# Optimization experiments

Measured on AMD Instinct MI355X. Metric: run time of the kernel, lower is better.

The kernel has to match this reference:

```python
import jax, jax.numpy as jnp
import numpy as np

R, S, D, V, K, B, L, U, I = 20000, 64, 128, 50000, 32, 2048, 20480, 100000, 100000


def setup_inputs() -> dict:
    key = jax.random.key(0)
    ks = jax.random.split(key, 16)
    # segment ids: equal-sized history per batch element (guaranteed non-empty)
    seg = (jnp.arange(L, dtype=jnp.int32) // (L // B)).astype(jnp.int32)
    return {
        "user": jax.random.randint(ks[0], (B,), 0, U, dtype=jnp.int32),
        "item": jax.random.randint(ks[1], (B,), 0, I, dtype=jnp.int32),
        "historical_review": jax.random.randint(ks[2], (R, S), 0, V, dtype=jnp.int32),
        "historical_review_positive": jax.random.normal(ks[3], (R, D), jnp.float32),
        "user_hist_idx": jax.random.randint(ks[4], (L,), 0, R, dtype=jnp.int32),
        "user_hist_seg": seg,
        "item_hist_idx": jax.random.randint(ks[5], (L,), 0, R, dtype=jnp.int32),
        "item_hist_seg": seg,
        "word_emb": jax.random.normal(ks[6], (V, D), jnp.float32) * 0.02,
        "M_w": jax.random.normal(ks[7], (D, D), jnp.float32) * (1.0 / np.sqrt(D)),
        "M_b": jnp.zeros((D,), jnp.float32),
        "W_w": jax.random.normal(ks[8], (D, K), jnp.float32) * (1.0 / np.sqrt(D)),
        "W_b": jnp.zeros((K,), jnp.float32),
        "T_w": jax.random.normal(ks[9], (K, D), jnp.float32) * (1.0 / np.sqrt(K)),
        "T_b": jnp.zeros((D,), jnp.float32),
        "user_emb": jax.random.normal(ks[10], (U, D), jnp.float32) * 0.02,
        "item_emb": jax.random.normal(ks[11], (I, D), jnp.float32) * 0.02,
        "avg_rating": jnp.full((1,), 3.5, jnp.float32),
    }


def _segment_mean(x, seg, num_segments):
    s = jax.ops.segment_sum(x, seg, num_segments=num_segments)
    c = jax.ops.segment_sum(jnp.ones(seg.shape, x.dtype), seg, num_segments=num_segments)
    return s / jnp.maximum(c, 1.0)[:, None]


def reference(user, item, historical_review, historical_review_positive,
              user_hist_idx, user_hist_seg, item_hist_idx, item_hist_seg,
              word_emb, M_w, M_b, W_w, W_b, T_w, T_b,
              user_emb, item_emb, avg_rating):
    # --- aspect extraction (ABAE-style) over R historical reviews ---
    e_w = word_emb[historical_review]                      # [R, S, D] gather
    y_s = historical_review_positive                       # [R, D] sentence embedding
    # dx = transform_M(e_w) @ y_s  -> attention logits over words
    dx = jnp.einsum('rsd,de,re->rs', e_w, M_w, y_s) + jnp.einsum('d,rd->r', M_b, y_s)[:, None]
    ax = jax.nn.softmax(dx, axis=1)                        # [R, S]
    z_s = jnp.einsum('rsd,rs->rd', e_w, ax)                # [R, D]
    p_t = jax.nn.softmax(z_s @ W_w + W_b, axis=1)          # [R, K] aspect probs
    r_s = p_t @ T_w + T_b                                  # [R, D] aspect-based review embedding
    # --- ragged gather + mean-pool over user/item histories ---
    ua = _segment_mean(r_s[user_hist_idx], user_hist_seg, B)  # [B, D]
    ia = _segment_mean(r_s[item_hist_idx], item_hist_seg, B)  # [B, D]
    uf = user_emb[user]                                    # [B, D]
    itf = item_emb[item]                                   # [B, D]
    prediction = jnp.sum(ua * ia, axis=-1) + jnp.sum(uf * itf, axis=-1) + avg_rating[0]
    return prediction  # [B]
```

## Files before the change

### kernel.cpp

```cpp
#include <hip/hip_runtime.h>


typedef __attribute__((ext_vector_type(8))) short bf16x8;
typedef __attribute__((ext_vector_type(4))) float f32x4;
typedef __attribute__((ext_vector_type(2))) float vf2;

__device__ __forceinline__ unsigned int f2bf_rne(float x) {
  unsigned int u = __float_as_uint(x);
  return (u + 0x7fffu + ((u >> 16) & 1u)) >> 16;
}

__global__ __launch_bounds__(256) void kA_mfma(
    const float* __restrict__ We, const float* __restrict__ Mw,
    const float* __restrict__ Ww, unsigned char* __restrict__ Z,
    int V, int ntiles) {
  __shared__ uint4 Bs[2560];
  int t = threadIdx.x;
  int L = t & 63, wid = t >> 6;

#pragma unroll
  for (int q = 0; q < 10; ++q) {
    int c = t + q * 256;
    int cl = c & 63, g = c >> 6;
    int jt = g >> 2, ks = g & 3;
    int n = jt * 16 + (cl & 15);
    int k0 = ks * 32 + (cl >> 4) * 8;
    float v[8];
#pragma unroll
    for (int j = 0; j < 8; ++j) {
      int e = k0 + j;
      v[j] = (n < 128) ? Mw[(size_t)e * 128 + n] : Ww[(size_t)e * 32 + (n - 128)];
    }
    uint4 pk;
    pk.x = f2bf_rne(v[0]) | (f2bf_rne(v[1]) << 16);
    pk.y = f2bf_rne(v[2]) | (f2bf_rne(v[3]) << 16);
    pk.z = f2bf_rne(v[4]) | (f2bf_rne(v[5]) << 16);
    pk.w = f2bf_rne(v[6]) | (f2bf_rne(v[7]) << 16);
    Bs[c] = pk;
  }
  __syncthreads();

  for (int tile = blockIdx.x; tile < ntiles; tile += gridDim.x) {
    int r0 = tile * 64;
    if (r0 > V - 64) r0 = V - 64;
    int rowA = r0 + wid * 16 + (L & 15);
    const float4* Arow = (const float4*)(We + (size_t)rowA * 128);

    f32x4 acc[10];
#pragma unroll
    for (int jt = 0; jt < 10; ++jt) acc[jt] = (f32x4){0.f, 0.f, 0.f, 0.f};

#pragma unroll
    for (int ks = 0; ks < 4; ++ks) {
      int koff4 = ks * 8 + (L >> 4) * 2;
      float4 a0 = Arow[koff4];
      float4 a1 = Arow[koff4 + 1];
      union { uint4 u; bf16x8 v; } A;
      A.u.x = f2bf_rne(a0.x) | (f2bf_rne(a0.y) << 16);
      A.u.y = f2bf_rne(a0.z) | (f2bf_rne(a0.w) << 16);
      A.u.z = f2bf_rne(a1.x) | (f2bf_rne(a1.y) << 16);
      A.u.w = f2bf_rne(a1.z) | (f2bf_rne(a1.w) << 16);
#pragma unroll
      for (int jt = 0; jt < 10; ++jt) {
        union { uint4 u; bf16x8 v; } Bf;
        Bf.u = Bs[(jt * 4 + ks) * 64 + L];
        acc[jt] = __builtin_amdgcn_mfma_f32_16x16x32_bf16(A.v, Bf.v, acc[jt], 0, 0, 0);
      }
    }

#pragma unroll
    for (int jt = 0; jt < 8; ++jt) {
#pragma unroll
      for (int i = 0; i < 4; ++i) {
        float v0 = acc[jt][i] * 64.f;
        float v1 = __shfl_xor(v0, 1);
        float v2 = __shfl_xor(v0, 2);
        float v3 = __shfl_xor(v0, 3);
        if (!(L & 3)) {
          int col = jt * 16 + (L & 15);
          int orow = r0 + wid * 16 + (L >> 4) * 4 + i;
          int w8 = __builtin_amdgcn_cvt_pk_fp8_f32(v0, v1, 0, false);
          w8 = __builtin_amdgcn_cvt_pk_fp8_f32(v2, v3, w8, true);
          *(int*)(Z + (size_t)orow * 192 + col) = w8;
        }
      }
    }
#pragma unroll
    for (int jt = 8; jt < 10; ++jt) {
#pragma unroll
      for (int i = 0; i < 4; ++i) {
        unsigned int u = f2bf_rne(acc[jt][i]);
        unsigned int partner = (unsigned int)__shfl_xor((int)u, 1);
        if (!(L & 1)) {
          int k = (jt - 8) * 16 + (L & 15);
          int orow = r0 + wid * 16 + (L >> 4) * 4 + i;
          *(unsigned int*)(Z + (size_t)orow * 192 + 128 + k * 2) = u | (partner << 16);
        }
      }
    }
  }
}

__device__ __forceinline__ float dot_fp8_16(uint4 q, const float4* y) {
  float s = 0.f;
#pragma unroll
  for (int i = 0; i < 4; ++i) {
    unsigned int u = (&q.x)[i];
    vf2 a = __builtin_amdgcn_cvt_pk_f32_fp8(u, false);
    vf2 b = __builtin_amdgcn_cvt_pk_f32_fp8(u, true);
    float4 yv = y[i];
    s += a.x * yv.x + a.y * yv.y + b.x * yv.z + b.y * yv.w;
  }
  return s;
}

__global__ __launch_bounds__(256) void k3_review(
    const int* __restrict__ hr, const float* __restrict__ Y,
    const unsigned char* __restrict__ Z, const float* __restrict__ Wb,
    const float* __restrict__ Tw, const float* __restrict__ Tb,
    float* __restrict__ rs, int R) {
  int t = threadIdx.x;
  int wv = t >> 6, lane = t & 63;
  int r = blockIdx.x * 4 + wv;
  if (r >= R) r = R - 1;

  int word = hr[(size_t)r * 64 + lane];
  int g = lane & 15, sub = lane >> 4;

  const float4* Yr = (const float4*)(Y + (size_t)r * 128);
  float4 ya[4], yb[4];
#pragma unroll
  for (int i = 0; i < 4; ++i) {
    ya[i] = Yr[sub * 4 + i];
    yb[i] = Yr[16 + sub * 4 + i];
  }

  const unsigned char* bp[4];
#pragma unroll
  for (int p = 0; p < 4; ++p) {
    int wid = __shfl(word, p * 16 + g);
    bp[p] = Z + (size_t)wid * 192 + sub * 16;
  }
  uint4 q0[4], q1[4];
#pragma unroll
  for (int p = 0; p < 4; ++p) {
    q0[p] = *(const uint4*)(bp[p]);
    q1[p] = *(const uint4*)(bp[p] + 64);
  }
  float dxp[4];
#pragma unroll
  for (int p = 0; p < 4; ++p) {
    float acc = dot_fp8_16(q0[p], ya) + dot_fp8_16(q1[p], yb);
    acc += __shfl_xor(acc, 16);
    acc += __shfl_xor(acc, 32);
    dxp[p] = acc * 0.015625f;
  }
  float dx = dxp[0];
  dx = (sub == 1) ? dxp[1] : dx;
  dx = (sub == 2) ? dxp[2] : dx;
  dx = (sub == 3) ? dxp[3] : dx;

  float m = dx;
#pragma unroll
  for (int off = 32; off; off >>= 1) m = fmaxf(m, __shfl_xor(m, off));
  float ex = __expf(dx - m);
  float sum = ex;
#pragma unroll
  for (int off = 32; off; off >>= 1) sum += __shfl_xor(sum, off);
  float ax = ex / sum;

  int k = lane & 31, half = lane >> 5;
  float lg = 0.f;
#pragma unroll 8
  for (int j = 0; j < 32; ++j) {
    int s = half * 32 + j;
    int wid_s = __shfl(word, s);
    float ax_s = __shfl(ax, s);
    unsigned short u = *(const unsigned short*)(Z + (size_t)wid_s * 192 + 128 + k * 2);
    lg += ax_s * __uint_as_float(((unsigned int)u) << 16);
  }
  lg += __shfl_xor(lg, 32);
  lg += Wb[k];
  float mk = lg;
#pragma unroll
  for (int off = 16; off; off >>= 1) mk = fmaxf(mk, __shfl_xor(mk, off));
  float ek = __expf(lg - mk);
  float sk = ek;
#pragma unroll
  for (int off = 16; off; off >>= 1) sk += __shfl_xor(sk, off);
  float p_own = ek / sk;

  const float2* T2 = (const float2*)Tw;
  float2 acc2 = ((const float2*)Tb)[lane];
#pragma unroll 8
  for (int kk = 0; kk < 32; ++kk) {
    float pk = __shfl(p_own, kk);
    float2 tv = T2[kk * 64 + lane];
    acc2.x += pk * tv.x;
    acc2.y += pk * tv.y;
  }
  ((float2*)rs)[(size_t)r * 64 + lane] = acc2;
}

__global__ __launch_bounds__(256) void k4_final(
    const float* __restrict__ rs, const int* __restrict__ uidx,
    const int* __restrict__ iidx, const int* __restrict__ user,
    const int* __restrict__ item, const float* __restrict__ uemb,
    const float* __restrict__ iemb, const float* __restrict__ avg,
    float* __restrict__ out, int B, int per) {
  int t = threadIdx.x;
  int w = t >> 6, lane = t & 63;
  int b = blockIdx.x * 4 + w;
  if (b >= B) return;
  const float2* rs2 = (const float2*)rs;
  float2 ua = {0.f, 0.f}, ia = {0.f, 0.f};
  int base = b * per;
  for (int j = 0; j < per; ++j) {
    int id = uidx[base + j];
    float2 tv = rs2[(size_t)id * 64 + lane];
    ua.x += tv.x; ua.y += tv.y;
  }
  for (int j = 0; j < per; ++j) {
    int id = iidx[base + j];
    float2 tv = rs2[(size_t)id * 64 + lane];
    ia.x += tv.x; ia.y += tv.y;
  }
  float inv = 1.0f / (float)per;
  float part = (ua.x * ia.x + ua.y * ia.y) * inv * inv;
  float2 uf = ((const float2*)uemb)[(size_t)user[b] * 64 + lane];
  float2 itf = ((const float2*)iemb)[(size_t)item[b] * 64 + lane];
  part += uf.x * itf.x + uf.y * itf.y;
#pragma unroll
  for (int off = 32; off; off >>= 1) part += __shfl_xor(part, off);
  if (lane == 0) out[b] = part + avg[0];
}

extern "C" void kernel_launch(void* const* d_in, const int* in_sizes, int n_in,
                              void* d_out, int out_size, void* d_ws, size_t ws_size,
                              hipStream_t stream) {
  const int*   user = (const int*)d_in[0];
  const int*   item = (const int*)d_in[1];
  const int*   hr   = (const int*)d_in[2];
  const float* Y    = (const float*)d_in[3];
  const int*   uhi  = (const int*)d_in[4];
  const int*   ihi  = (const int*)d_in[6];
  const float* We   = (const float*)d_in[8];
  const float* Mw   = (const float*)d_in[9];
  const float* Ww   = (const float*)d_in[11];
  const float* Wb   = (const float*)d_in[12];
  const float* Tw   = (const float*)d_in[13];
  const float* Tb   = (const float*)d_in[14];
  const float* Ue   = (const float*)d_in[15];
  const float* Ie   = (const float*)d_in[16];
  const float* avg  = (const float*)d_in[17];

  int B = in_sizes[0];
  int R = in_sizes[3] / 128;
  int V = in_sizes[8] / 128;
  int L = in_sizes[4];
  int per = L / B;

  unsigned char* Z = (unsigned char*)d_ws;
  float* rsbuf = (float*)(Z + (size_t)V * 192);
  float* out = (float*)d_out;

  int ntiles = (V + 63) / 64;
  int ka_grid = (ntiles + 2) / 3;
  kA_mfma<<<ka_grid, 256, 0, stream>>>(We, Mw, Ww, Z, V, ntiles);
  k3_review<<<(R + 3) / 4, 256, 0, stream>>>(hr, Y, Z, Wb, Tw, Tb, rsbuf, R);
  k4_final<<<(B + 3) / 4, 256, 0, stream>>>(rsbuf, uhi, ihi, user, item, Ue, Ie, avg, out, B, per);
}
```

Before: 254.2 us.

## Vectorize aspect-logit gather in review kernel and use one tile per block in precompute

In the review kernel, the bf16 W-projection part of each word row is now loaded as one 16-byte vector per lane, alongside the fp8 M part, and issued before the Y loads. The aspect logits are then accumulated per lane over 8 aspects and reduced with shuffles, replacing 32 serial 2-byte dependent gathers per word. This removes many small scattered loads and long dependency chains, at the cost of more registers and shuffle reductions. The precompute kernel also drops its grid-stride loop and launches one block per 64-row tile, which restages the LDS weights in every block in exchange for more parallelism.

```diff
diff --git a/kernel.cpp b/kernel.cpp
--- a/kernel.cpp
+++ b/kernel.cpp
@@ -9,11 +9,12 @@
   unsigned int u = __float_as_uint(x);
   return (u + 0x7fffu + ((u >> 16) & 1u)) >> 16;
 }
+__device__ __forceinline__ float bf_lo(unsigned int w) { return __uint_as_float(w << 16); }
+__device__ __forceinline__ float bf_hi(unsigned int w) { return __uint_as_float(w & 0xffff0000u); }
 
 __global__ __launch_bounds__(256) void kA_mfma(
     const float* __restrict__ We, const float* __restrict__ Mw,
-    const float* __restrict__ Ww, unsigned char* __restrict__ Z,
-    int V, int ntiles) {
+    const float* __restrict__ Ww, unsigned char* __restrict__ Z, int V) {
   __shared__ uint4 Bs[2560];
   int t = threadIdx.x;
   int L = t & 63, wid = t >> 6;
@@ -40,62 +41,60 @@
   }
   __syncthreads();
 
-  for (int tile = blockIdx.x; tile < ntiles; tile += gridDim.x) {
-    int r0 = tile * 64;
-    if (r0 > V - 64) r0 = V - 64;
-    int rowA = r0 + wid * 16 + (L & 15);
-    const float4* Arow = (const float4*)(We + (size_t)rowA * 128);
-
-    f32x4 acc[10];
-#pragma unroll
-    for (int jt = 0; jt < 10; ++jt) acc[jt] = (f32x4){0.f, 0.f, 0.f, 0.f};
-
-#pragma unroll
-    for (int ks = 0; ks < 4; ++ks) {
-      int koff4 = ks * 8 + (L >> 4) * 2;
-      float4 a0 = Arow[koff4];
-      float4 a1 = Arow[koff4 + 1];
-      union { uint4 u; bf16x8 v; } A;
-      A.u.x = f2bf_rne(a0.x) | (f2bf_rne(a0.y) << 16);
-      A.u.y = f2bf_rne(a0.z) | (f2bf_rne(a0.w) << 16);
-      A.u.z = f2bf_rne(a1.x) | (f2bf_rne(a1.y) << 16);
-      A.u.w = f2bf_rne(a1.z) | (f2bf_rne(a1.w) << 16);
-#pragma unroll
-      for (int jt = 0; jt < 10; ++jt) {
-        union { uint4 u; bf16x8 v; } Bf;
-        Bf.u = Bs[(jt * 4 + ks) * 64 + L];
-        acc[jt] = __builtin_amdgcn_mfma_f32_16x16x32_bf16(A.v, Bf.v, acc[jt], 0, 0, 0);
+  int r0 = blockIdx.x * 64;
+  if (r0 > V - 64) r0 = V - 64;
+  int rowA = r0 + wid * 16 + (L & 15);
+  const float4* Arow = (const float4*)(We + (size_t)rowA * 128);
+
+  f32x4 acc[10];
+#pragma unroll
+  for (int jt = 0; jt < 10; ++jt) acc[jt] = (f32x4){0.f, 0.f, 0.f, 0.f};
+
+#pragma unroll
+  for (int ks = 0; ks < 4; ++ks) {
+    int koff4 = ks * 8 + (L >> 4) * 2;
+    float4 a0 = Arow[koff4];
+    float4 a1 = Arow[koff4 + 1];
+    union { uint4 u; bf16x8 v; } A;
+    A.u.x = f2bf_rne(a0.x) | (f2bf_rne(a0.y) << 16);
+    A.u.y = f2bf_rne(a0.z) | (f2bf_rne(a0.w) << 16);
+    A.u.z = f2bf_rne(a1.x) | (f2bf_rne(a1.y) << 16);
+    A.u.w = f2bf_rne(a1.z) | (f2bf_rne(a1.w) << 16);
+#pragma unroll
+    for (int jt = 0; jt < 10; ++jt) {
+      union { uint4 u; bf16x8 v; } Bf;
+      Bf.u = Bs[(jt * 4 + ks) * 64 + L];
+      acc[jt] = __builtin_amdgcn_mfma_f32_16x16x32_bf16(A.v, Bf.v, acc[jt], 0, 0, 0);
+    }
+  }
+
+#pragma unroll
+  for (int jt = 0; jt < 8; ++jt) {
+#pragma unroll
+    for (int i = 0; i < 4; ++i) {
+      float v0 = acc[jt][i] * 64.f;
+      float v1 = __shfl_xor(v0, 1);
+      float v2 = __shfl_xor(v0, 2);
+      float v3 = __shfl_xor(v0, 3);
+      if (!(L & 3)) {
+        int col = jt * 16 + (L & 15);
+        int orow = r0 + wid * 16 + (L >> 4) * 4 + i;
+        int w8 = __builtin_amdgcn_cvt_pk_fp8_f32(v0, v1, 0, false);
+        w8 = __builtin_amdgcn_cvt_pk_fp8_f32(v2, v3, w8, true);
+        *(int*)(Z + (size_t)orow * 192 + col) = w8;
       }
     }
-
-#pragma unroll
-    for (int jt = 0; jt < 8; ++jt) {
-#pragma unroll
-      for (int i = 0; i < 4; ++i) {
-        float v0 = acc[jt][i] * 64.f;
-        float v1 = __shfl_xor(v0, 1);
-        float v2 = __shfl_xor(v0, 2);
-        float v3 = __shfl_xor(v0, 3);
-        if (!(L & 3)) {
-          int col = jt * 16 + (L & 15);
-          int orow = r0 + wid * 16 + (L >> 4) * 4 + i;
-          int w8 = __builtin_amdgcn_cvt_pk_fp8_f32(v0, v1, 0, false);
-          w8 = __builtin_amdgcn_cvt_pk_fp8_f32(v2, v3, w8, true);
-          *(int*)(Z + (size_t)orow * 192 + col) = w8;
-        }
-      }
-    }
-#pragma unroll
-    for (int jt = 8; jt < 10; ++jt) {
-#pragma unroll
-      for (int i = 0; i < 4; ++i) {
-        unsigned int u = f2bf_rne(acc[jt][i]);
-        unsigned int partner = (unsigned int)__shfl_xor((int)u, 1);
-        if (!(L & 1)) {
-          int k = (jt - 8) * 16 + (L & 15);
-          int orow = r0 + wid * 16 + (L >> 4) * 4 + i;
-          *(unsigned int*)(Z + (size_t)orow * 192 + 128 + k * 2) = u | (partner << 16);
-        }
+  }
+#pragma unroll
+  for (int jt = 8; jt < 10; ++jt) {
+#pragma unroll
+    for (int i = 0; i < 4; ++i) {
+      unsigned int u = f2bf_rne(acc[jt][i]);
+      unsigned int partner = (unsigned int)__shfl_xor((int)u, 1);
+      if (!(L & 1)) {
+        int k = (jt - 8) * 16 + (L & 15);
+        int orow = r0 + wid * 16 + (L >> 4) * 4 + i;
+        *(unsigned int*)(Z + (size_t)orow * 192 + 128 + k * 2) = u | (partner << 16);
       }
     }
   }
@@ -127,6 +126,19 @@
   int word = hr[(size_t)r * 64 + lane];
   int g = lane & 15, sub = lane >> 4;
 
+  const unsigned char* bp[4];
+#pragma unroll
+  for (int p = 0; p < 4; ++p) {
+    int wid = __shfl(word, p * 16 + g);
+    bp[p] = Z + (size_t)wid * 192;
+  }
+  uint4 q0[4], q1[4], w8[4];
+#pragma unroll
+  for (int p = 0; p < 4; ++p) {
+    q0[p] = *(const uint4*)(bp[p] + sub * 16);
+    q1[p] = *(const uint4*)(bp[p] + 64 + sub * 16);
+    w8[p] = *(const uint4*)(bp[p] + 128 + sub * 16);
+  }
   const float4* Yr = (const float4*)(Y + (size_t)r * 128);
   float4 ya[4], yb[4];
 #pragma unroll
@@ -135,18 +147,6 @@
     yb[i] = Yr[16 + sub * 4 + i];
   }
 
-  const unsigned char* bp[4];
-#pragma unroll
-  for (int p = 0; p < 4; ++p) {
-    int wid = __shfl(word, p * 16 + g);
-    bp[p] = Z + (size_t)wid * 192 + sub * 16;
-  }
-  uint4 q0[4], q1[4];
-#pragma unroll
-  for (int p = 0; p < 4; ++p) {
-    q0[p] = *(const uint4*)(bp[p]);
-    q1[p] = *(const uint4*)(bp[p] + 64);
-  }
   float dxp[4];
 #pragma unroll
   for (int p = 0; p < 4; ++p) {
@@ -169,32 +169,49 @@
   for (int off = 32; off; off >>= 1) sum += __shfl_xor(sum, off);
   float ax = ex / sum;
 
-  int k = lane & 31, half = lane >> 5;
-  float lg = 0.f;
-#pragma unroll 8
-  for (int j = 0; j < 32; ++j) {
-    int s = half * 32 + j;
-    int wid_s = __shfl(word, s);
-    float ax_s = __shfl(ax, s);
-    unsigned short u = *(const unsigned short*)(Z + (size_t)wid_s * 192 + 128 + k * 2);
-    lg += ax_s * __uint_as_float(((unsigned int)u) << 16);
-  }
-  lg += __shfl_xor(lg, 32);
-  lg += Wb[k];
-  float mk = lg;
-#pragma unroll
-  for (int off = 16; off; off >>= 1) mk = fmaxf(mk, __shfl_xor(mk, off));
-  float ek = __expf(lg - mk);
-  float sk = ek;
-#pragma unroll
-  for (int off = 16; off; off >>= 1) sk += __shfl_xor(sk, off);
-  float p_own = ek / sk;
+  float lacc[8];
+#pragma unroll
+  for (int j = 0; j < 8; ++j) lacc[j] = 0.f;
+#pragma unroll
+  for (int p = 0; p < 4; ++p) {
+    float axp = __shfl(ax, p * 16 + g);
+#pragma unroll
+    for (int j = 0; j < 8; ++j) {
+      unsigned int u = (&w8[p].x)[j >> 1];
+      float wwv = (j & 1) ? bf_hi(u) : bf_lo(u);
+      lacc[j] += axp * wwv;
+    }
+  }
+#pragma unroll
+  for (int off = 8; off; off >>= 1) {
+#pragma unroll
+    for (int j = 0; j < 8; ++j) lacc[j] += __shfl_xor(lacc[j], off);
+  }
+  const float4* Wb4 = (const float4*)Wb;
+  float4 wba = Wb4[sub * 2], wbb = Wb4[sub * 2 + 1];
+  lacc[0] += wba.x; lacc[1] += wba.y; lacc[2] += wba.z; lacc[3] += wba.w;
+  lacc[4] += wbb.x; lacc[5] += wbb.y; lacc[6] += wbb.z; lacc[7] += wbb.w;
+
+  float mk = lacc[0];
+#pragma unroll
+  for (int j = 1; j < 8; ++j) mk = fmaxf(mk, lacc[j]);
+  mk = fmaxf(mk, __shfl_xor(mk, 16));
+  mk = fmaxf(mk, __shfl_xor(mk, 32));
+  float ek[8], sk = 0.f;
+#pragma unroll
+  for (int j = 0; j < 8; ++j) { ek[j] = __expf(lacc[j] - mk); sk += ek[j]; }
+  sk += __shfl_xor(sk, 16);
+  sk += __shfl_xor(sk, 32);
+  float inv = 1.0f / sk;
+  float pv[8];
+#pragma unroll
+  for (int j = 0; j < 8; ++j) pv[j] = ek[j] * inv;
 
   const float2* T2 = (const float2*)Tw;
   float2 acc2 = ((const float2*)Tb)[lane];
-#pragma unroll 8
+#pragma unroll
   for (int kk = 0; kk < 32; ++kk) {
-    float pk = __shfl(p_own, kk);
+    float pk = __shfl(pv[kk & 7], (kk >> 3) * 16);
     float2 tv = T2[kk * 64 + lane];
     acc2.x += pk * tv.x;
     acc2.y += pk * tv.y;
@@ -264,9 +281,7 @@
   float* rsbuf = (float*)(Z + (size_t)V * 192);
   float* out = (float*)d_out;
 
-  int ntiles = (V + 63) / 64;
-  int ka_grid = (ntiles + 2) / 3;
-  kA_mfma<<<ka_grid, 256, 0, stream>>>(We, Mw, Ww, Z, V, ntiles);
+  kA_mfma<<<(V + 63) / 64, 256, 0, stream>>>(We, Mw, Ww, Z, V);
   k3_review<<<(R + 3) / 4, 256, 0, stream>>>(hr, Y, Z, Wb, Tw, Tb, rsbuf, R);
   k4_final<<<(B + 3) / 4, 256, 0, stream>>>(rsbuf, uhi, ihi, user, item, Ue, Ie, avg, out, B, per);
 }
```

New measurement: 238.0 us. -6.4%, faster.
